# Optimization experiments

Hardware: AMD Instinct MI355X
Metric: run time of the kernel (lower is better)

Reference implementation:

```python
import jax, jax.numpy as jnp
import numpy as np

EMBED_DIM = 256
NUM_HEADS = 8
WINDOW = 64
HEAD_DIM = EMBED_DIM // NUM_HEADS


def setup_inputs() -> dict:
    key = jax.random.key(0)
    k_x, k_w, k_ow = jax.random.split(key, 3)
    B, S, E = 2, 4096, EMBED_DIM
    x = jax.random.normal(k_x, (B, S, E), dtype=jnp.float32)
    # nn.MultiheadAttention params: packed in_proj (q,k,v) and out_proj
    bound = 1.0 / np.sqrt(E)
    in_proj_w = jax.random.uniform(k_w, (3 * E, E), jnp.float32, -bound, bound)
    in_proj_b = jnp.zeros((3 * E,), jnp.float32)
    out_w = jax.random.uniform(k_ow, (E, E), jnp.float32, -bound, bound)
    out_b = jnp.zeros((E,), jnp.float32)
    return {"x": x, "in_proj_w": in_proj_w, "in_proj_b": in_proj_b,
            "out_w": out_w, "out_b": out_b}


def reference(x, in_proj_w, in_proj_b, out_w, out_b):
    B, S, E = x.shape
    H, D = NUM_HEADS, HEAD_DIM
    # packed qkv projection (torch Linear: y = x @ W^T + b)
    qkv = jnp.einsum('bse,fe->bsf', x, in_proj_w) + in_proj_b  # [B,S,3E]
    q, k, v = jnp.split(qkv, 3, axis=-1)
    q = q.reshape(B, S, H, D).transpose(0, 2, 1, 3)  # [B,H,S,D]
    k = k.reshape(B, S, H, D).transpose(0, 2, 1, 3)
    v = v.reshape(B, S, H, D).transpose(0, 2, 1, 3)
    scale = 1.0 / jnp.sqrt(jnp.asarray(D, x.dtype))
    scores = jnp.einsum('bhqd,bhkd->bhqk', q * scale, k)  # [B,H,S,S]
    idx = jnp.arange(S)
    band = jnp.abs(idx[:, None] - idx[None, :]) <= WINDOW  # [S,S]
    neg = jnp.asarray(-1e9, scores.dtype)
    scores = jnp.where(band[None, None, :, :], scores, neg)
    attn = jax.nn.softmax(scores, axis=-1)
    out = jnp.einsum('bhqk,bhkd->bhqd', attn, v)  # [B,H,S,D]
    out = out.transpose(0, 2, 1, 3).reshape(B, S, E)
    return jnp.einsum('bse,fe->bsf', out, out_w) + out_b
```

## Files before the change

### kernel.cpp

```cpp
#include <hip/hip_runtime.h>
#include <hip/hip_bf16.h>

#define S_LEN 4096
#define EMB   256
#define NHEAD 8
#define HDIM  32
#define WIN   64
#define BATCH 2

typedef __attribute__((ext_vector_type(8))) short short8;
typedef __attribute__((ext_vector_type(4))) float floatx4;
typedef unsigned short u16;
typedef unsigned int   u32;

static __device__ __forceinline__ u32 bf16_rn(float x) {
    u32 u = __float_as_uint(x);
    return (u + 0x7FFFu + ((u >> 16) & 1u)) >> 16;
}
static __device__ __forceinline__ u32 packsplit(float x) {
    const u32 hi = bf16_rn(x);
    const float hf = __uint_as_float(hi << 16);
    const u32 lo = bf16_rn(x - hf);
    return (hi << 16) | lo;
}
static __device__ __forceinline__ void unpack_pair(u32 p0, u32 p1, u32& h, u32& l) {
    h = (p0 >> 16) | (p1 & 0xFFFF0000u);
    l = (p0 & 0xFFFFu) | (p1 << 16);
}
static __device__ __forceinline__ void unpack8(uint4 a, uint4 b, uint4& h, uint4& l) {
    unpack_pair(a.x, a.y, h.x, l.x);
    unpack_pair(a.z, a.w, h.y, l.y);
    unpack_pair(b.x, b.y, h.z, l.z);
    unpack_pair(b.z, b.w, h.w, l.w);
}

#define NX4 524288
#define NW4 49152
#define NO4 16384

__global__ __launch_bounds__(256) void convert_kernel(
    const float* __restrict__ X, const float* __restrict__ Wi, const float* __restrict__ Wo,
    u32* __restrict__ Xp, u32* __restrict__ Wip, u32* __restrict__ Wop)
{
    const int i = blockIdx.x * 256 + threadIdx.x;
    const float* src; u32* dst; int off;
    if (i < NX4)            { src = X;  dst = Xp;  off = i; }
    else if (i < NX4 + NW4) { src = Wi; dst = Wip; off = i - NX4; }
    else                    { src = Wo; dst = Wop; off = i - NX4 - NW4; }
    const float4 v = *(const float4*)(src + (size_t)off * 4);
    uint4 o;
    o.x = packsplit(v.x); o.y = packsplit(v.y);
    o.z = packsplit(v.z); o.w = packsplit(v.w);
    *(uint4*)(dst + (size_t)off * 4) = o;
}

#define LDA 40

__global__ __launch_bounds__(256) void qkv_proj_kernel(
    const u32* __restrict__ Xp, const u32* __restrict__ Wp,
    const float* __restrict__ bias,
    u32* __restrict__ Qp, u32* __restrict__ Kp, u32* __restrict__ Vp)
{
    __shared__ __align__(16) u16 Ah[128 * LDA], Al[128 * LDA];
    __shared__ __align__(16) u16 Bh[64 * LDA],  Bl[64 * LDA];
    const int tid = threadIdx.x;
    const int m0 = blockIdx.y * 128, n0 = blockIdx.x * 64;
    const int srow = tid >> 2, sc = tid & 3;
    const int lane = tid & 63, wv = tid >> 6;
    const int wm = (wv >> 1) * 64, wn = (wv & 1) * 32;
    const int lm = lane & 15, kq = lane >> 4;

    uint4 pA[2][2], pB[2];
#pragma unroll
    for (int r = 0; r < 2; ++r) {
        const u32* base = Xp + (size_t)(m0 + srow + r * 64) * EMB + sc * 8;
        pA[r][0] = *(const uint4*)base;
        pA[r][1] = *(const uint4*)(base + 4);
    }
    {
        const u32* base = Wp + (size_t)(n0 + srow) * EMB + sc * 8;
        pB[0] = *(const uint4*)base;
        pB[1] = *(const uint4*)(base + 4);
    }

    floatx4 acc[4][2] = {};
    for (int t = 0; t < 8; ++t) {
        __syncthreads();
#pragma unroll
        for (int r = 0; r < 2; ++r) {
            uint4 h, l;
            unpack8(pA[r][0], pA[r][1], h, l);
            *(uint4*)&Ah[(srow + r * 64) * LDA + sc * 8] = h;
            *(uint4*)&Al[(srow + r * 64) * LDA + sc * 8] = l;
        }
        {
            uint4 h, l;
            unpack8(pB[0], pB[1], h, l);
            *(uint4*)&Bh[srow * LDA + sc * 8] = h;
            *(uint4*)&Bl[srow * LDA + sc * 8] = l;
        }
        __syncthreads();
        if (t < 7) {
            const int k0 = (t + 1) * 32;
#pragma unroll
            for (int r = 0; r < 2; ++r) {
                const u32* base = Xp + (size_t)(m0 + srow + r * 64) * EMB + k0 + sc * 8;
                pA[r][0] = *(const uint4*)base;
                pA[r][1] = *(const uint4*)(base + 4);
            }
            const u32* base = Wp + (size_t)(n0 + srow) * EMB + k0 + sc * 8;
            pB[0] = *(const uint4*)base;
            pB[1] = *(const uint4*)(base + 4);
        }
        short8 a_h[4], a_l[4], b_h[2], b_l[2];
#pragma unroll
        for (int mt = 0; mt < 4; ++mt) {
            a_h[mt] = *(const short8*)&Ah[(wm + mt * 16 + lm) * LDA + kq * 8];
            a_l[mt] = *(const short8*)&Al[(wm + mt * 16 + lm) * LDA + kq * 8];
        }
#pragma unroll
        for (int nt = 0; nt < 2; ++nt) {
            b_h[nt] = *(const short8*)&Bh[(wn + nt * 16 + lm) * LDA + kq * 8];
            b_l[nt] = *(const short8*)&Bl[(wn + nt * 16 + lm) * LDA + kq * 8];
        }
#pragma unroll
        for (int mt = 0; mt < 4; ++mt)
#pragma unroll
            for (int nt = 0; nt < 2; ++nt) {
                acc[mt][nt] = __builtin_amdgcn_mfma_f32_16x16x32_bf16(a_h[mt], b_h[nt], acc[mt][nt], 0, 0, 0);
                acc[mt][nt] = __builtin_amdgcn_mfma_f32_16x16x32_bf16(a_h[mt], b_l[nt], acc[mt][nt], 0, 0, 0);
                acc[mt][nt] = __builtin_amdgcn_mfma_f32_16x16x32_bf16(a_l[mt], b_h[nt], acc[mt][nt], 0, 0, 0);
            }
    }
#pragma unroll
    for (int nt = 0; nt < 2; ++nt) {
        const int f = n0 + wn + nt * 16 + lm;
        const int which = f >> 8;
        const int h = (f & 255) >> 5, d = f & 31;
        u32* dst = (which == 0) ? Qp : ((which == 1) ? Kp : Vp);
        const float sc2 = (which == 0) ? 0.17677669529663687f : 1.0f;
        const float bf = bias[f];
#pragma unroll
        for (int mt = 0; mt < 4; ++mt)
#pragma unroll
            for (int r = 0; r < 4; ++r) {
                const int m = m0 + wm + mt * 16 + kq * 4 + r;
                const int b = m >> 12, s = m & (S_LEN - 1);
                dst[(((size_t)b * NHEAD + h) * S_LEN + s) * HDIM + d]
                    = packsplit((acc[mt][nt][r] + bf) * sc2);
            }
    }
}

__global__ __launch_bounds__(256) void out_proj_kernel(
    const u32* __restrict__ Abp, const u32* __restrict__ Wp,
    const float* __restrict__ bias, float* __restrict__ C)
{
    __shared__ __align__(16) u16 Ah[128 * LDA], Al[128 * LDA];
    __shared__ __align__(16) u16 Bh[64 * LDA],  Bl[64 * LDA];
    const int tid = threadIdx.x;
    const int m0 = blockIdx.y * 128, n0 = blockIdx.x * 64;
    const int srow = tid >> 2, sc = tid & 3;
    const int lane = tid & 63, wv = tid >> 6;
    const int wm = (wv >> 1) * 64, wn = (wv & 1) * 32;
    const int lm = lane & 15, kq = lane >> 4;

    uint4 pA[2][2], pB[2];
#pragma unroll
    for (int r = 0; r < 2; ++r) {
        const u32* base = Abp + (size_t)(m0 + srow + r * 64) * EMB + sc * 8;
        pA[r][0] = *(const uint4*)base;
        pA[r][1] = *(const uint4*)(base + 4);
    }
    {
        const u32* base = Wp + (size_t)(n0 + srow) * EMB + sc * 8;
        pB[0] = *(const uint4*)base;
        pB[1] = *(const uint4*)(base + 4);
    }

    floatx4 acc[4][2] = {};
    for (int t = 0; t < 8; ++t) {
        __syncthreads();
#pragma unroll
        for (int r = 0; r < 2; ++r) {
            uint4 h, l;
            unpack8(pA[r][0], pA[r][1], h, l);
            *(uint4*)&Ah[(srow + r * 64) * LDA + sc * 8] = h;
            *(uint4*)&Al[(srow + r * 64) * LDA + sc * 8] = l;
        }
        {
            uint4 h, l;
            unpack8(pB[0], pB[1], h, l);
            *(uint4*)&Bh[srow * LDA + sc * 8] = h;
            *(uint4*)&Bl[srow * LDA + sc * 8] = l;
        }
        __syncthreads();
        if (t < 7) {
            const int k0 = (t + 1) * 32;
#pragma unroll
            for (int r = 0; r < 2; ++r) {
                const u32* base = Abp + (size_t)(m0 + srow + r * 64) * EMB + k0 + sc * 8;
                pA[r][0] = *(const uint4*)base;
                pA[r][1] = *(const uint4*)(base + 4);
            }
            const u32* base = Wp + (size_t)(n0 + srow) * EMB + k0 + sc * 8;
            pB[0] = *(const uint4*)base;
            pB[1] = *(const uint4*)(base + 4);
        }
        short8 a_h[4], a_l[4], b_h[2], b_l[2];
#pragma unroll
        for (int mt = 0; mt < 4; ++mt) {
            a_h[mt] = *(const short8*)&Ah[(wm + mt * 16 + lm) * LDA + kq * 8];
            a_l[mt] = *(const short8*)&Al[(wm + mt * 16 + lm) * LDA + kq * 8];
        }
#pragma unroll
        for (int nt = 0; nt < 2; ++nt) {
            b_h[nt] = *(const short8*)&Bh[(wn + nt * 16 + lm) * LDA + kq * 8];
            b_l[nt] = *(const short8*)&Bl[(wn + nt * 16 + lm) * LDA + kq * 8];
        }
#pragma unroll
        for (int mt = 0; mt < 4; ++mt)
#pragma unroll
            for (int nt = 0; nt < 2; ++nt) {
                acc[mt][nt] = __builtin_amdgcn_mfma_f32_16x16x32_bf16(a_h[mt], b_h[nt], acc[mt][nt], 0, 0, 0);
                acc[mt][nt] = __builtin_amdgcn_mfma_f32_16x16x32_bf16(a_h[mt], b_l[nt], acc[mt][nt], 0, 0, 0);
                acc[mt][nt] = __builtin_amdgcn_mfma_f32_16x16x32_bf16(a_l[mt], b_h[nt], acc[mt][nt], 0, 0, 0);
            }
    }
#pragma unroll
    for (int nt = 0; nt < 2; ++nt) {
        const int f = n0 + wn + nt * 16 + lm;
        const float bf = bias[f];
#pragma unroll
        for (int mt = 0; mt < 4; ++mt)
#pragma unroll
            for (int r = 0; r < 4; ++r) {
                const int m = m0 + wm + mt * 16 + kq * 4 + r;
                C[(size_t)m * EMB + f] = acc[mt][nt][r] + bf;
            }
    }
}

#define AKS 40
#define AVS 200
#define APS 200

__global__ __launch_bounds__(256) void local_attn_kernel(
    const u32* __restrict__ Qp, const u32* __restrict__ Kp,
    const u32* __restrict__ Vp, u32* __restrict__ Abp)
{
    __shared__ __align__(16) u16 Qh[64 * AKS], Ql[64 * AKS];
    __shared__ __align__(16) u16 Kh[192 * AKS], Kl[192 * AKS];
    __shared__ __align__(16) u16 Vt[32 * AVS];
    __shared__ __align__(16) u16 Pw[4 * 16 * APS];

    const int tid = threadIdx.x;
    const int q0 = blockIdx.x * 64;
    const int h = blockIdx.y, b = blockIdx.z;
    const int jmin = max(0, q0 - WIN);
    const int jmax = min(S_LEN - 1, q0 + 63 + WIN);
    const int nk = jmax - jmin + 1;
    const size_t bhS = ((size_t)b * NHEAD + h) * S_LEN;
    const size_t qoff = (bhS + q0) * HDIM;
    const size_t koff = (bhS + jmin) * HDIM;

    const int srow = tid >> 2, sc = tid & 3;
    {
        const u32* base = Qp + qoff + (size_t)srow * HDIM + sc * 8;
        uint4 h4, l4;
        unpack8(*(const uint4*)base, *(const uint4*)(base + 4), h4, l4);
        *(uint4*)&Qh[srow * AKS + sc * 8] = h4;
        *(uint4*)&Ql[srow * AKS + sc * 8] = l4;
    }
#pragma unroll
    for (int r = 0; r < 3; ++r) {
        const int t = srow + r * 64;
        const int tc = min(t, nk - 1);
        const u32* base = Kp + koff + (size_t)tc * HDIM + sc * 8;
        uint4 h4, l4;
        unpack8(*(const uint4*)base, *(const uint4*)(base + 4), h4, l4);
        *(uint4*)&Kh[t * AKS + sc * 8] = h4;
        *(uint4*)&Kl[t * AKS + sc * 8] = l4;
    }
#pragma unroll
    for (int r = 0; r < 3; ++r) {
        const int t = srow + r * 64;
        const int tc = min(t, nk - 1);
        const u32* base = Vp + koff + (size_t)tc * HDIM + sc * 8;
        const uint4 v0 = *(const uint4*)base;
        const uint4 v1 = *(const uint4*)(base + 4);
        const int d0 = sc * 8;
        Vt[(d0 + 0) * AVS + t] = (u16)(v0.x >> 16);
        Vt[(d0 + 1) * AVS + t] = (u16)(v0.y >> 16);
        Vt[(d0 + 2) * AVS + t] = (u16)(v0.z >> 16);
        Vt[(d0 + 3) * AVS + t] = (u16)(v0.w >> 16);
        Vt[(d0 + 4) * AVS + t] = (u16)(v1.x >> 16);
        Vt[(d0 + 5) * AVS + t] = (u16)(v1.y >> 16);
        Vt[(d0 + 6) * AVS + t] = (u16)(v1.z >> 16);
        Vt[(d0 + 7) * AVS + t] = (u16)(v1.w >> 16);
    }
    __syncthreads();

    const int lane = tid & 63, wv = tid >> 6;
    const int lm = lane & 15, quad = lane >> 4;
    const int qbase = wv * 16;

    const short8 qh = *(const short8*)&Qh[(qbase + lm) * AKS + quad * 8];
    const short8 ql = *(const short8*)&Ql[(qbase + lm) * AKS + quad * 8];

    floatx4 sacc[12];
#pragma unroll
    for (int nt = 0; nt < 12; ++nt) {
        const short8 bh = *(const short8*)&Kh[(nt * 16 + lm) * AKS + quad * 8];
        const short8 bl = *(const short8*)&Kl[(nt * 16 + lm) * AKS + quad * 8];
        floatx4 a = {};
        a = __builtin_amdgcn_mfma_f32_16x16x32_bf16(qh, bh, a, 0, 0, 0);
        a = __builtin_amdgcn_mfma_f32_16x16x32_bf16(qh, bl, a, 0, 0, 0);
        a = __builtin_amdgcn_mfma_f32_16x16x32_bf16(ql, bh, a, 0, 0, 0);
        sacc[nt] = a;
    }

    const int qg = q0 + qbase + quad * 4;
    float mx[4] = {-1e30f, -1e30f, -1e30f, -1e30f};
#pragma unroll
    for (int nt = 0; nt < 12; ++nt) {
        const int slot = nt * 16 + lm;
        const int keyg = jmin + slot;
#pragma unroll
        for (int r = 0; r < 4; ++r) {
            const int qr = qg + r;
            const bool valid = (slot < nk) && (keyg >= qr - WIN) && (keyg <= qr + WIN);
            const float sv = valid ? sacc[nt][r] : -1e30f;
            sacc[nt][r] = sv;
            mx[r] = fmaxf(mx[r], sv);
        }
    }
#pragma unroll
    for (int r = 0; r < 4; ++r) {
        mx[r] = fmaxf(mx[r], __shfl_xor(mx[r], 1));
        mx[r] = fmaxf(mx[r], __shfl_xor(mx[r], 2));
        mx[r] = fmaxf(mx[r], __shfl_xor(mx[r], 4));
        mx[r] = fmaxf(mx[r], __shfl_xor(mx[r], 8));
    }
    float l[4] = {0.f, 0.f, 0.f, 0.f};
    u16* Pme = &Pw[wv * 16 * APS];
#pragma unroll
    for (int nt = 0; nt < 12; ++nt)
#pragma unroll
        for (int r = 0; r < 4; ++r) {
            const float p = __expf(sacc[nt][r] - mx[r]);
            l[r] += p;
            Pme[(quad * 4 + r) * APS + nt * 16 + lm] = (u16)bf16_rn(p);
        }
#pragma unroll
    for (int r = 0; r < 4; ++r) {
        l[r] += __shfl_xor(l[r], 1);
        l[r] += __shfl_xor(l[r], 2);
        l[r] += __shfl_xor(l[r], 4);
        l[r] += __shfl_xor(l[r], 8);
    }
    const float rl[4] = {1.f / l[0], 1.f / l[1], 1.f / l[2], 1.f / l[3]};

    floatx4 oacc[2] = {};
#pragma unroll
    for (int ks = 0; ks < 6; ++ks) {
        const short8 ap  = *(const short8*)&Pme[lm * APS + ks * 32 + quad * 8];
        const short8 bv0 = *(const short8*)&Vt[lm * AVS + ks * 32 + quad * 8];
        const short8 bv1 = *(const short8*)&Vt[(16 + lm) * AVS + ks * 32 + quad * 8];
        oacc[0] = __builtin_amdgcn_mfma_f32_16x16x32_bf16(ap, bv0, oacc[0], 0, 0, 0);
        oacc[1] = __builtin_amdgcn_mfma_f32_16x16x32_bf16(ap, bv1, oacc[1], 0, 0, 0);
    }
#pragma unroll
    for (int nt = 0; nt < 2; ++nt)
#pragma unroll
        for (int r = 0; r < 4; ++r) {
            const int qrow = qbase + quad * 4 + r;
            Abp[((size_t)b * S_LEN + q0 + qrow) * EMB + h * HDIM + nt * 16 + lm]
                = packsplit(oacc[nt][r] * rl[r]);
        }
}

extern "C" void kernel_launch(void* const* d_in, const int* in_sizes, int n_in,
                              void* d_out, int out_size, void* d_ws, size_t ws_size,
                              hipStream_t stream) {
    const float* x  = (const float*)d_in[0];
    const float* wi = (const float*)d_in[1];
    const float* bi = (const float*)d_in[2];
    const float* wo = (const float*)d_in[3];
    const float* bo = (const float*)d_in[4];
    float* out = (float*)d_out;

    const size_t per = (size_t)BATCH * NHEAD * S_LEN * HDIM;
    u32* p = (u32*)d_ws;
    u32* Xp  = p; p += per;
    u32* Wip = p; p += 768 * EMB;
    u32* Wop = p; p += EMB * EMB;
    u32* Qp  = p; p += per;
    u32* Kp  = p; p += per;
    u32* Vp  = p; p += per;
    u32* Abp = p; p += per;

    convert_kernel<<<dim3((NX4 + NW4 + NO4) / 256), 256, 0, stream>>>(
        x, wi, wo, Xp, Wip, Wop);
    qkv_proj_kernel<<<dim3(768 / 64, 8192 / 128), 256, 0, stream>>>(
        Xp, Wip, bi, Qp, Kp, Vp);
    local_attn_kernel<<<dim3(S_LEN / 64, NHEAD, BATCH), 256, 0, stream>>>(
        Qp, Kp, Vp, Abp);
    out_proj_kernel<<<dim3(256 / 64, 8192 / 128), 256, 0, stream>>>(
        Abp, Wop, bo, out);
}
```

Before: 112.7 us.

## Fuse fp32-to-split-bf16 conversion into GEMM loads and trim attention key band

Removes the standalone convert kernel: the QKV and output projection kernels now read fp32 inputs and weights directly and split them into hi/lo bf16 while staging into shared memory. This drops one launch and the round trip of writing and re-reading packed copies of X and the weights. In the attention kernel each wave now processes only the 144 keys relevant to its 16 queries, offset by a per-wave base, instead of all 192. That cuts the QK and PV MFMA work and the exp count, and the P and V shared-memory strides change to fit. In exchange the split arithmetic is redone per tile, once per column block, and there is extra padding and zeroing logic in the P buffer.

```diff
diff --git a/kernel.cpp b/kernel.cpp
--- a/kernel.cpp
+++ b/kernel.cpp
@@ -23,6 +23,21 @@
     const u32 lo = bf16_rn(x - hf);
     return (hi << 16) | lo;
 }
+static __device__ __forceinline__ void split2(float x, u32& hi, u32& lo) {
+    hi = bf16_rn(x);
+    const float hf = __uint_as_float(hi << 16);
+    lo = bf16_rn(x - hf);
+}
+static __device__ __forceinline__ void split_store4(u16* hp, u16* lp, float4 v) {
+    u32 h0, l0, h1, l1, h2, l2, h3, l3;
+    split2(v.x, h0, l0); split2(v.y, h1, l1);
+    split2(v.z, h2, l2); split2(v.w, h3, l3);
+    uint2 hv, lv;
+    hv.x = h0 | (h1 << 16); hv.y = h2 | (h3 << 16);
+    lv.x = l0 | (l1 << 16); lv.y = l2 | (l3 << 16);
+    *(uint2*)hp = hv;
+    *(uint2*)lp = lv;
+}
 static __device__ __forceinline__ void unpack_pair(u32 p0, u32 p1, u32& h, u32& l) {
     h = (p0 >> 16) | (p1 & 0xFFFF0000u);
     l = (p0 & 0xFFFFu) | (p1 << 16);
@@ -34,30 +49,10 @@
     unpack_pair(b.z, b.w, h.w, l.w);
 }
 
-#define NX4 524288
-#define NW4 49152
-#define NO4 16384
-
-__global__ __launch_bounds__(256) void convert_kernel(
-    const float* __restrict__ X, const float* __restrict__ Wi, const float* __restrict__ Wo,
-    u32* __restrict__ Xp, u32* __restrict__ Wip, u32* __restrict__ Wop)
-{
-    const int i = blockIdx.x * 256 + threadIdx.x;
-    const float* src; u32* dst; int off;
-    if (i < NX4)            { src = X;  dst = Xp;  off = i; }
-    else if (i < NX4 + NW4) { src = Wi; dst = Wip; off = i - NX4; }
-    else                    { src = Wo; dst = Wop; off = i - NX4 - NW4; }
-    const float4 v = *(const float4*)(src + (size_t)off * 4);
-    uint4 o;
-    o.x = packsplit(v.x); o.y = packsplit(v.y);
-    o.z = packsplit(v.z); o.w = packsplit(v.w);
-    *(uint4*)(dst + (size_t)off * 4) = o;
-}
-
 #define LDA 40
 
 __global__ __launch_bounds__(256) void qkv_proj_kernel(
-    const u32* __restrict__ Xp, const u32* __restrict__ Wp,
+    const float* __restrict__ X, const float* __restrict__ W,
     const float* __restrict__ bias,
     u32* __restrict__ Qp, u32* __restrict__ Kp, u32* __restrict__ Vp)
 {
@@ -65,52 +60,37 @@
     __shared__ __align__(16) u16 Bh[64 * LDA],  Bl[64 * LDA];
     const int tid = threadIdx.x;
     const int m0 = blockIdx.y * 128, n0 = blockIdx.x * 64;
-    const int srow = tid >> 2, sc = tid & 3;
+    const int r0 = tid >> 3, c4 = tid & 7;
     const int lane = tid & 63, wv = tid >> 6;
     const int wm = (wv >> 1) * 64, wn = (wv & 1) * 32;
     const int lm = lane & 15, kq = lane >> 4;
 
-    uint4 pA[2][2], pB[2];
-#pragma unroll
-    for (int r = 0; r < 2; ++r) {
-        const u32* base = Xp + (size_t)(m0 + srow + r * 64) * EMB + sc * 8;
-        pA[r][0] = *(const uint4*)base;
-        pA[r][1] = *(const uint4*)(base + 4);
-    }
-    {
-        const u32* base = Wp + (size_t)(n0 + srow) * EMB + sc * 8;
-        pB[0] = *(const uint4*)base;
-        pB[1] = *(const uint4*)(base + 4);
-    }
+    float4 ar[4], wr[2];
+#pragma unroll
+    for (int r = 0; r < 4; ++r)
+        ar[r] = *(const float4*)(X + (size_t)(m0 + r0 + r * 32) * EMB + c4 * 4);
+#pragma unroll
+    for (int r = 0; r < 2; ++r)
+        wr[r] = *(const float4*)(W + (size_t)(n0 + r0 + r * 32) * EMB + c4 * 4);
 
     floatx4 acc[4][2] = {};
     for (int t = 0; t < 8; ++t) {
         __syncthreads();
 #pragma unroll
-        for (int r = 0; r < 2; ++r) {
-            uint4 h, l;
-            unpack8(pA[r][0], pA[r][1], h, l);
-            *(uint4*)&Ah[(srow + r * 64) * LDA + sc * 8] = h;
-            *(uint4*)&Al[(srow + r * 64) * LDA + sc * 8] = l;
-        }
-        {
-            uint4 h, l;
-            unpack8(pB[0], pB[1], h, l);
-            *(uint4*)&Bh[srow * LDA + sc * 8] = h;
-            *(uint4*)&Bl[srow * LDA + sc * 8] = l;
-        }
+        for (int r = 0; r < 4; ++r)
+            split_store4(&Ah[(r0 + r * 32) * LDA + c4 * 4], &Al[(r0 + r * 32) * LDA + c4 * 4], ar[r]);
+#pragma unroll
+        for (int r = 0; r < 2; ++r)
+            split_store4(&Bh[(r0 + r * 32) * LDA + c4 * 4], &Bl[(r0 + r * 32) * LDA + c4 * 4], wr[r]);
         __syncthreads();
         if (t < 7) {
             const int k0 = (t + 1) * 32;
 #pragma unroll
-            for (int r = 0; r < 2; ++r) {
-                const u32* base = Xp + (size_t)(m0 + srow + r * 64) * EMB + k0 + sc * 8;
-                pA[r][0] = *(const uint4*)base;
-                pA[r][1] = *(const uint4*)(base + 4);
-            }
-            const u32* base = Wp + (size_t)(n0 + srow) * EMB + k0 + sc * 8;
-            pB[0] = *(const uint4*)base;
-            pB[1] = *(const uint4*)(base + 4);
+            for (int r = 0; r < 4; ++r)
+                ar[r] = *(const float4*)(X + (size_t)(m0 + r0 + r * 32) * EMB + k0 + c4 * 4);
+#pragma unroll
+            for (int r = 0; r < 2; ++r)
+                wr[r] = *(const float4*)(W + (size_t)(n0 + r0 + r * 32) * EMB + k0 + c4 * 4);
         }
         short8 a_h[4], a_l[4], b_h[2], b_l[2];
 #pragma unroll
@@ -153,7 +133,7 @@
 }
 
 __global__ __launch_bounds__(256) void out_proj_kernel(
-    const u32* __restrict__ Abp, const u32* __restrict__ Wp,
+    const u32* __restrict__ Abp, const float* __restrict__ W,
     const float* __restrict__ bias, float* __restrict__ C)
 {
     __shared__ __align__(16) u16 Ah[128 * LDA], Al[128 * LDA];
@@ -161,21 +141,19 @@
     const int tid = threadIdx.x;
     const int m0 = blockIdx.y * 128, n0 = blockIdx.x * 64;
     const int srow = tid >> 2, sc = tid & 3;
+    const int r0 = tid >> 3, c4 = tid & 7;
     const int lane = tid & 63, wv = tid >> 6;
     const int wm = (wv >> 1) * 64, wn = (wv & 1) * 32;
     const int lm = lane & 15, kq = lane >> 4;
 
-    uint4 pA[2][2], pB[2];
+    uint4 pA[2][2];
+    float4 wr[2];
 #pragma unroll
     for (int r = 0; r < 2; ++r) {
         const u32* base = Abp + (size_t)(m0 + srow + r * 64) * EMB + sc * 8;
         pA[r][0] = *(const uint4*)base;
         pA[r][1] = *(const uint4*)(base + 4);
-    }
-    {
-        const u32* base = Wp + (size_t)(n0 + srow) * EMB + sc * 8;
-        pB[0] = *(const uint4*)base;
-        pB[1] = *(const uint4*)(base + 4);
+        wr[r] = *(const float4*)(W + (size_t)(n0 + r0 + r * 32) * EMB + c4 * 4);
     }
 
     floatx4 acc[4][2] = {};
@@ -187,12 +165,7 @@
             unpack8(pA[r][0], pA[r][1], h, l);
             *(uint4*)&Ah[(srow + r * 64) * LDA + sc * 8] = h;
             *(uint4*)&Al[(srow + r * 64) * LDA + sc * 8] = l;
-        }
-        {
-            uint4 h, l;
-            unpack8(pB[0], pB[1], h, l);
-            *(uint4*)&Bh[srow * LDA + sc * 8] = h;
-            *(uint4*)&Bl[srow * LDA + sc * 8] = l;
+            split_store4(&Bh[(r0 + r * 32) * LDA + c4 * 4], &Bl[(r0 + r * 32) * LDA + c4 * 4], wr[r]);
         }
         __syncthreads();
         if (t < 7) {
@@ -202,10 +175,8 @@
                 const u32* base = Abp + (size_t)(m0 + srow + r * 64) * EMB + k0 + sc * 8;
                 pA[r][0] = *(const uint4*)base;
                 pA[r][1] = *(const uint4*)(base + 4);
-            }
-            const u32* base = Wp + (size_t)(n0 + srow) * EMB + k0 + sc * 8;
-            pB[0] = *(const uint4*)base;
-            pB[1] = *(const uint4*)(base + 4);
+                wr[r] = *(const float4*)(W + (size_t)(n0 + r0 + r * 32) * EMB + k0 + c4 * 4);
+            }
         }
         short8 a_h[4], a_l[4], b_h[2], b_l[2];
 #pragma unroll
@@ -242,8 +213,8 @@
 }
 
 #define AKS 40
-#define AVS 200
-#define APS 200
+#define AVS 224
+#define APS 160
 
 __global__ __launch_bounds__(256) void local_attn_kernel(
     const u32* __restrict__ Qp, const u32* __restrict__ Kp,
@@ -283,36 +254,40 @@
         *(uint4*)&Kl[t * AKS + sc * 8] = l4;
     }
 #pragma unroll
-    for (int r = 0; r < 3; ++r) {
+    for (int r = 0; r < 4; ++r) {
         const int t = srow + r * 64;
-        const int tc = min(t, nk - 1);
-        const u32* base = Vp + koff + (size_t)tc * HDIM + sc * 8;
-        const uint4 v0 = *(const uint4*)base;
-        const uint4 v1 = *(const uint4*)(base + 4);
-        const int d0 = sc * 8;
-        Vt[(d0 + 0) * AVS + t] = (u16)(v0.x >> 16);
-        Vt[(d0 + 1) * AVS + t] = (u16)(v0.y >> 16);
-        Vt[(d0 + 2) * AVS + t] = (u16)(v0.z >> 16);
-        Vt[(d0 + 3) * AVS + t] = (u16)(v0.w >> 16);
-        Vt[(d0 + 4) * AVS + t] = (u16)(v1.x >> 16);
-        Vt[(d0 + 5) * AVS + t] = (u16)(v1.y >> 16);
-        Vt[(d0 + 6) * AVS + t] = (u16)(v1.z >> 16);
-        Vt[(d0 + 7) * AVS + t] = (u16)(v1.w >> 16);
+        if (t < 224) {
+            const int tc = min(t, nk - 1);
+            const u32* base = Vp + koff + (size_t)tc * HDIM + sc * 8;
+            const uint4 v0 = *(const uint4*)base;
+            const uint4 v1 = *(const uint4*)(base + 4);
+            const int d0 = sc * 8;
+            Vt[(d0 + 0) * AVS + t] = (u16)(v0.x >> 16);
+            Vt[(d0 + 1) * AVS + t] = (u16)(v0.y >> 16);
+            Vt[(d0 + 2) * AVS + t] = (u16)(v0.z >> 16);
+            Vt[(d0 + 3) * AVS + t] = (u16)(v0.w >> 16);
+            Vt[(d0 + 4) * AVS + t] = (u16)(v1.x >> 16);
+            Vt[(d0 + 5) * AVS + t] = (u16)(v1.y >> 16);
+            Vt[(d0 + 6) * AVS + t] = (u16)(v1.z >> 16);
+            Vt[(d0 + 7) * AVS + t] = (u16)(v1.w >> 16);
+        }
     }
     __syncthreads();
 
     const int lane = tid & 63, wv = tid >> 6;
     const int lm = lane & 15, quad = lane >> 4;
     const int qbase = wv * 16;
+    const int sbase = max(0, qbase + q0 - WIN - jmin);
 
     const short8 qh = *(const short8*)&Qh[(qbase + lm) * AKS + quad * 8];
     const short8 ql = *(const short8*)&Ql[(qbase + lm) * AKS + quad * 8];
 
-    floatx4 sacc[12];
-#pragma unroll
-    for (int nt = 0; nt < 12; ++nt) {
-        const short8 bh = *(const short8*)&Kh[(nt * 16 + lm) * AKS + quad * 8];
-        const short8 bl = *(const short8*)&Kl[(nt * 16 + lm) * AKS + quad * 8];
+    floatx4 sacc[9];
+#pragma unroll
+    for (int nt = 0; nt < 9; ++nt) {
+        const int srow2 = sbase + nt * 16 + lm;
+        const short8 bh = *(const short8*)&Kh[srow2 * AKS + quad * 8];
+        const short8 bl = *(const short8*)&Kl[srow2 * AKS + quad * 8];
         floatx4 a = {};
         a = __builtin_amdgcn_mfma_f32_16x16x32_bf16(qh, bh, a, 0, 0, 0);
         a = __builtin_amdgcn_mfma_f32_16x16x32_bf16(qh, bl, a, 0, 0, 0);
@@ -323,8 +298,8 @@
     const int qg = q0 + qbase + quad * 4;
     float mx[4] = {-1e30f, -1e30f, -1e30f, -1e30f};
 #pragma unroll
-    for (int nt = 0; nt < 12; ++nt) {
-        const int slot = nt * 16 + lm;
+    for (int nt = 0; nt < 9; ++nt) {
+        const int slot = sbase + nt * 16 + lm;
         const int keyg = jmin + slot;
 #pragma unroll
         for (int r = 0; r < 4; ++r) {
@@ -345,13 +320,17 @@
     float l[4] = {0.f, 0.f, 0.f, 0.f};
     u16* Pme = &Pw[wv * 16 * APS];
 #pragma unroll
-    for (int nt = 0; nt < 12; ++nt)
+    for (int nt = 0; nt < 9; ++nt)
 #pragma unroll
         for (int r = 0; r < 4; ++r) {
             const float p = __expf(sacc[nt][r] - mx[r]);
             l[r] += p;
             Pme[(quad * 4 + r) * APS + nt * 16 + lm] = (u16)bf16_rn(p);
         }
+    {
+        uint2 z; z.x = 0u; z.y = 0u;
+        *(uint2*)&Pme[(lane >> 2) * APS + 144 + (lane & 3) * 4] = z;
+    }
 #pragma unroll
     for (int r = 0; r < 4; ++r) {
         l[r] += __shfl_xor(l[r], 1);
@@ -363,10 +342,10 @@
 
     floatx4 oacc[2] = {};
 #pragma unroll
-    for (int ks = 0; ks < 6; ++ks) {
+    for (int ks = 0; ks < 5; ++ks) {
         const short8 ap  = *(const short8*)&Pme[lm * APS + ks * 32 + quad * 8];
-        const short8 bv0 = *(const short8*)&Vt[lm * AVS + ks * 32 + quad * 8];
-        const short8 bv1 = *(const short8*)&Vt[(16 + lm) * AVS + ks * 32 + quad * 8];
+        const short8 bv0 = *(const short8*)&Vt[lm * AVS + sbase + ks * 32 + quad * 8];
+        const short8 bv1 = *(const short8*)&Vt[(16 + lm) * AVS + sbase + ks * 32 + quad * 8];
         oacc[0] = __builtin_amdgcn_mfma_f32_16x16x32_bf16(ap, bv0, oacc[0], 0, 0, 0);
         oacc[1] = __builtin_amdgcn_mfma_f32_16x16x32_bf16(ap, bv1, oacc[1], 0, 0, 0);
     }
@@ -392,20 +371,15 @@
 
     const size_t per = (size_t)BATCH * NHEAD * S_LEN * HDIM;
     u32* p = (u32*)d_ws;
-    u32* Xp  = p; p += per;
-    u32* Wip = p; p += 768 * EMB;
-    u32* Wop = p; p += EMB * EMB;
     u32* Qp  = p; p += per;
     u32* Kp  = p; p += per;
     u32* Vp  = p; p += per;
     u32* Abp = p; p += per;
 
-    convert_kernel<<<dim3((NX4 + NW4 + NO4) / 256), 256, 0, stream>>>(
-        x, wi, wo, Xp, Wip, Wop);
     qkv_proj_kernel<<<dim3(768 / 64, 8192 / 128), 256, 0, stream>>>(
-        Xp, Wip, bi, Qp, Kp, Vp);
+        x, wi, bi, Qp, Kp, Vp);
     local_attn_kernel<<<dim3(S_LEN / 64, NHEAD, BATCH), 256, 0, stream>>>(
         Qp, Kp, Vp, Abp);
     out_proj_kernel<<<dim3(256 / 64, 8192 / 128), 256, 0, stream>>>(
-        Abp, Wop, bo, out);
-}
+        Abp, wo, bo, out);
+}
```

Measured after the change: 114.6 us. No clear change (+1.6%).
